# Optimization experiments

Hardware: AMD Instinct MI355X
Metric: run time of the kernel (lower is better)

The kernel has to match this reference:

```python
import jax, jax.numpy as jnp
import numpy as np

IN_FEATURES = 4096
OUT_FEATURES = 4096
LORA_R = 64
LORA_ALPHA = 16
SCALING = LORA_ALPHA / LORA_R  # 0.25


def setup_inputs() -> dict:
    key = jax.random.key(0)
    k_x, k_w, k_s, k_a, k_b = jax.random.split(key, 5)
    x = jax.random.normal(k_x, (4, 2048, IN_FEATURES), dtype=jnp.float32)
    # int8 quantized base weight in [-8, 7] as in the torch buffer init
    weight_quantized = jax.random.randint(k_w, (OUT_FEATURES, IN_FEATURES), -8, 7, dtype=jnp.int8)
    weight_scale = jax.random.normal(k_s, (1,), dtype=jnp.float32)
    lora_A = jax.random.normal(k_a, (LORA_R, IN_FEATURES), dtype=jnp.float32) * 0.01
    # torch init is zeros; use small random values so the LoRA path is exercised
    lora_B = jax.random.normal(k_b, (OUT_FEATURES, LORA_R), dtype=jnp.float32) * 0.01
    return {"x": x, "weight_quantized": weight_quantized, "weight_scale": weight_scale,
            "lora_A": lora_A, "lora_B": lora_B}


def reference(x, weight_quantized, weight_scale, lora_A, lora_B):
    # 1. dequantize base weight on the fly: [out, in]
    w_dequant = weight_quantized.astype(x.dtype) * weight_scale
    # 2. base GEMM: [B, S, in] x [in, out] -> [B, S, out]
    base = jnp.einsum('bsi,oi->bso', x, w_dequant)
    # 3. LoRA low-rank update (dropout is identity in eval mode)
    lora = jnp.einsum('bsr,or->bso', jnp.einsum('bsi,ri->bsr', x, lora_A), lora_B)
    return base + lora * SCALING
```

## Files before the change

### kernel.cpp

```cpp
#include <hip/hip_runtime.h>

#define M_TOT 8192
#define K_TOT 4096
#define N_TOT 4096
#define RANK  64
#define SCALING 0.25f

typedef __bf16 bf16x8 __attribute__((ext_vector_type(8)));
typedef float floatx4 __attribute__((ext_vector_type(4)));

static __device__ __forceinline__ unsigned short f32_to_bf16(float f) {
  unsigned int u = __float_as_uint(f);
  u += 0x7FFFu + ((u >> 16) & 1u);
  return (unsigned short)(u >> 16);
}

static __device__ __forceinline__ void async_ld16(const void* g, void* l) {
  __builtin_amdgcn_global_load_lds(
      (const __attribute__((address_space(1))) unsigned int*)g,
      (__attribute__((address_space(3))) unsigned int*)l, 16, 0, 0);
}

__global__ __launch_bounds__(256) void cvt_x_kernel(const float4* __restrict__ x,
                                                    ushort4* __restrict__ xb) {
  int i = blockIdx.x * 256 + threadIdx.x;
  float4 v = x[i];
  ushort4 o;
  o.x = f32_to_bf16(v.x);
  o.y = f32_to_bf16(v.y);
  o.z = f32_to_bf16(v.z);
  o.w = f32_to_bf16(v.w);
  xb[i] = o;
}

__global__ __launch_bounds__(256) void prep_kernel(
    const int* __restrict__ wq, const float* __restrict__ scale_p,
    const float* __restrict__ A, const float* __restrict__ B,
    unsigned short* __restrict__ Weff, unsigned short* __restrict__ Ab,
    unsigned short* __restrict__ Bb) {
  const int blk = blockIdx.x;
  const int tid = threadIdx.x;
  if (blk < 16384) {
    const float scale = scale_p[0];
    const size_t i = (size_t)(blk * 256 + tid) * 4;
    const int4 wv = *(const int4*)(wq + i);
    ushort4 st;
    st.x = f32_to_bf16((float)wv.x * scale);
    st.y = f32_to_bf16((float)wv.y * scale);
    st.z = f32_to_bf16((float)wv.z * scale);
    st.w = f32_to_bf16((float)wv.w * scale);
    *(ushort4*)(Weff + i) = st;
  } else if (blk < 16640) {
    const size_t i = (size_t)((blk - 16384) * 256 + tid) * 4;
    const float4 v = *(const float4*)(A + i);
    ushort4 st;
    st.x = f32_to_bf16(v.x);
    st.y = f32_to_bf16(v.y);
    st.z = f32_to_bf16(v.z);
    st.w = f32_to_bf16(v.w);
    *(ushort4*)(Ab + i) = st;
  } else {
    const size_t i = (size_t)((blk - 16640) * 256 + tid) * 4;
    const float4 v = *(const float4*)(B + i);
    ushort4 st;
    st.x = f32_to_bf16(v.x * SCALING);
    st.y = f32_to_bf16(v.y * SCALING);
    st.z = f32_to_bf16(v.z * SCALING);
    st.w = f32_to_bf16(v.w * SCALING);
    *(ushort4*)(Bb + i) = st;
  }
}

__global__ __launch_bounds__(256) void lora_y_kernel(
    const unsigned short* __restrict__ Xb,
    const unsigned short* __restrict__ Ab,
    unsigned short* __restrict__ Yb) {
  __shared__ __align__(16) unsigned short Xs[2 * 64 * 32];
  __shared__ __align__(16) unsigned short As[2 * 64 * 32];

  const int tid = threadIdx.x;
  const int lane = tid & 63;
  const int wave = tid >> 6;
  const int m0 = blockIdx.x * 64;

  const int sRow = tid >> 2;
  const int sCol = (tid & 3) * 8;
  const unsigned short* xg = Xb + (size_t)(m0 + sRow) * K_TOT + sCol;
  const unsigned short* ag = Ab + (size_t)sRow * K_TOT + sCol;
  unsigned short* lx0 = Xs + tid * 8;
  unsigned short* lx1 = Xs + 64 * 32 + tid * 8;
  unsigned short* la0 = As + tid * 8;
  unsigned short* la1 = As + 64 * 32 + tid * 8;

  const unsigned short* px = Xs + (wave * 16 + (lane & 15)) * 32 + (lane >> 4) * 8;
  const unsigned short* pav = As + (lane & 15) * 32 + (lane >> 4) * 8;

  floatx4 acc[4] = {};
  for (int kt = 0; kt < K_TOT; kt += 64) {
    __syncthreads();
    async_ld16(xg + kt, lx0);
    async_ld16(xg + kt + 32, lx1);
    async_ld16(ag + kt, la0);
    async_ld16(ag + kt + 32, la1);
    __syncthreads();
#pragma unroll
    for (int ks = 0; ks < 2; ++ks) {
      bf16x8 xf = *(const bf16x8*)(px + ks * 64 * 32);
#pragma unroll
      for (int j = 0; j < 4; ++j) {
        bf16x8 af = *(const bf16x8*)(pav + ks * 64 * 32 + j * 16 * 32);
        acc[j] = __builtin_amdgcn_mfma_f32_16x16x32_bf16(xf, af, acc[j], 0, 0, 0);
      }
    }
  }
  const int row0 = m0 + wave * 16 + ((lane >> 4) << 2);
  const int col0 = lane & 15;
#pragma unroll
  for (int j = 0; j < 4; ++j)
#pragma unroll
    for (int r = 0; r < 4; ++r)
      Yb[(size_t)(row0 + r) * RANK + (col0 + j * 16)] = f32_to_bf16(acc[j][r]);
}

__global__ __launch_bounds__(256) void gemm_kernel(
    const unsigned short* __restrict__ Xb,
    const unsigned short* __restrict__ Wb,
    const unsigned short* __restrict__ Yb,
    const unsigned short* __restrict__ Bb,
    float* __restrict__ out) {
  __shared__ __align__(16) unsigned short As[2 * 128 * 32];
  __shared__ __align__(16) unsigned short Bs[2 * 128 * 32];

  const int tid = threadIdx.x;
  const int lane = tid & 63;
  const int wave = tid >> 6;
  const int wm = wave >> 1;
  const int wn = wave & 1;

  const int bM = blockIdx.y * 128;
  const int bN = blockIdx.x * 128;

  const int sRow = tid >> 2;
  const int sCol = (tid & 3) * 8;
  const unsigned short* xg0 = Xb + (size_t)(bM + sRow) * K_TOT + sCol;
  const unsigned short* xg1 = xg0 + (size_t)64 * K_TOT;
  const unsigned short* wg0 = Wb + (size_t)(bN + sRow) * K_TOT + sCol;
  const unsigned short* wg1 = wg0 + (size_t)64 * K_TOT;
  unsigned short* la00 = As + tid * 8;
  unsigned short* la01 = As + 64 * 32 + tid * 8;
  unsigned short* la10 = As + 128 * 32 + tid * 8;
  unsigned short* la11 = As + 128 * 32 + 64 * 32 + tid * 8;
  unsigned short* lb00 = Bs + tid * 8;
  unsigned short* lb01 = Bs + 64 * 32 + tid * 8;
  unsigned short* lb10 = Bs + 128 * 32 + tid * 8;
  unsigned short* lb11 = Bs + 128 * 32 + 64 * 32 + tid * 8;

  const unsigned short* pa = As + ((wm * 64) + (lane & 15)) * 32 + (lane >> 4) * 8;
  const unsigned short* pb = Bs + ((wn * 64) + (lane & 15)) * 32 + (lane >> 4) * 8;

  floatx4 acc[4][4] = {};

  for (int kt = 0; kt < K_TOT; kt += 64) {
    __syncthreads();
    async_ld16(xg0 + kt, la00);
    async_ld16(xg1 + kt, la01);
    async_ld16(xg0 + kt + 32, la10);
    async_ld16(xg1 + kt + 32, la11);
    async_ld16(wg0 + kt, lb00);
    async_ld16(wg1 + kt, lb01);
    async_ld16(wg0 + kt + 32, lb10);
    async_ld16(wg1 + kt + 32, lb11);
    __syncthreads();

#pragma unroll
    for (int ks = 0; ks < 2; ++ks) {
      const unsigned short* pak = pa + ks * 128 * 32;
      const unsigned short* pbk = pb + ks * 128 * 32;
      bf16x8 af[4], bf[4];
#pragma unroll
      for (int i = 0; i < 4; ++i) af[i] = *(const bf16x8*)(pak + i * 16 * 32);
#pragma unroll
      for (int j = 0; j < 4; ++j) bf[j] = *(const bf16x8*)(pbk + j * 16 * 32);
#pragma unroll
      for (int i = 0; i < 4; ++i)
#pragma unroll
        for (int j = 0; j < 4; ++j)
          acc[i][j] = __builtin_amdgcn_mfma_f32_16x16x32_bf16(af[i], bf[j], acc[i][j], 0, 0, 0);
    }
  }

  {
    const unsigned short* yg0 = Yb + (size_t)(bM + sRow) * RANK + sCol;
    const unsigned short* yg1 = yg0 + (size_t)64 * RANK;
    const unsigned short* bg0 = Bb + (size_t)(bN + sRow) * RANK + sCol;
    const unsigned short* bg1 = bg0 + (size_t)64 * RANK;
    __syncthreads();
    async_ld16(yg0, la00);
    async_ld16(yg1, la01);
    async_ld16(yg0 + 32, la10);
    async_ld16(yg1 + 32, la11);
    async_ld16(bg0, lb00);
    async_ld16(bg1, lb01);
    async_ld16(bg0 + 32, lb10);
    async_ld16(bg1 + 32, lb11);
    __syncthreads();
#pragma unroll
    for (int ks = 0; ks < 2; ++ks) {
      const unsigned short* pak = pa + ks * 128 * 32;
      const unsigned short* pbk = pb + ks * 128 * 32;
      bf16x8 af[4], bf[4];
#pragma unroll
      for (int i = 0; i < 4; ++i) af[i] = *(const bf16x8*)(pak + i * 16 * 32);
#pragma unroll
      for (int j = 0; j < 4; ++j) bf[j] = *(const bf16x8*)(pbk + j * 16 * 32);
#pragma unroll
      for (int i = 0; i < 4; ++i)
#pragma unroll
        for (int j = 0; j < 4; ++j)
          acc[i][j] = __builtin_amdgcn_mfma_f32_16x16x32_bf16(af[i], bf[j], acc[i][j], 0, 0, 0);
    }
  }

  const int row0 = bM + wm * 64 + ((lane >> 4) << 2);
  const int col0 = bN + wn * 64 + (lane & 15);
#pragma unroll
  for (int i = 0; i < 4; ++i)
#pragma unroll
    for (int j = 0; j < 4; ++j)
#pragma unroll
      for (int r = 0; r < 4; ++r)
        out[(size_t)(row0 + i * 16 + r) * N_TOT + (col0 + j * 16)] = acc[i][j][r];
}

extern "C" void kernel_launch(void* const* d_in, const int* in_sizes, int n_in,
                              void* d_out, int out_size, void* d_ws, size_t ws_size,
                              hipStream_t stream) {
  const float* x      = (const float*)d_in[0];
  const int*   wq     = (const int*)d_in[1];
  const float* wscale = (const float*)d_in[2];
  const float* lora_A = (const float*)d_in[3];
  const float* lora_B = (const float*)d_in[4];
  float* out = (float*)d_out;

  char* ws = (char*)d_ws;
  unsigned short* xb   = (unsigned short*)(ws);
  unsigned short* weff = (unsigned short*)(ws + 67108864);
  unsigned short* yb   = (unsigned short*)(ws + 100663296);
  unsigned short* ab   = (unsigned short*)(ws + 101711872);
  unsigned short* bb   = (unsigned short*)(ws + 102236160);

  cvt_x_kernel<<<32768, 256, 0, stream>>>((const float4*)x, (ushort4*)xb);
  prep_kernel<<<16896, 256, 0, stream>>>(wq, wscale, lora_A, lora_B, weff, ab, bb);
  lora_y_kernel<<<128, 256, 0, stream>>>(xb, ab, yb);
  gemm_kernel<<<dim3(N_TOT / 128, M_TOT / 128), 256, 0, stream>>>(xb, weff, yb, bb, out);
}
```

Measured before the change: 606.2 us.

## Fuse x bf16 conversion into LoRA down-projection kernel and swizzle GEMM tiles

The standalone fp32-to-bf16 conversion of x is folded into the LoRA x·A^T kernel. That kernel now reads fp32 x once, converts it in registers, writes bf16 x to LDS and to global for the main GEMM, and prefetches the next chunk, which removes a separate 128MB read pass. The LoRA kernel uses 32-row tiles (256 blocks instead of 128) to spread work across more CUs. The main GEMM switches to a 1D grid with grouped tile ordering (32 M-tiles per group) to improve L2 reuse of the weight and x tiles. The fused kernel still runs only 256 blocks and its global stores are not async, so the conversion may be limited by that low parallelism.

New measurement: 596.4 us. Within noise of the previous version (-1.6%).

```diff
diff --git a/kernel.cpp b/kernel.cpp
--- a/kernel.cpp
+++ b/kernel.cpp
@@ -8,6 +8,7 @@
 
 typedef __bf16 bf16x8 __attribute__((ext_vector_type(8)));
 typedef float floatx4 __attribute__((ext_vector_type(4)));
+typedef unsigned short ushort8 __attribute__((ext_vector_type(8)));
 
 static __device__ __forceinline__ unsigned short f32_to_bf16(float f) {
   unsigned int u = __float_as_uint(f);
@@ -19,18 +20,6 @@
   __builtin_amdgcn_global_load_lds(
       (const __attribute__((address_space(1))) unsigned int*)g,
       (__attribute__((address_space(3))) unsigned int*)l, 16, 0, 0);
-}
-
-__global__ __launch_bounds__(256) void cvt_x_kernel(const float4* __restrict__ x,
-                                                    ushort4* __restrict__ xb) {
-  int i = blockIdx.x * 256 + threadIdx.x;
-  float4 v = x[i];
-  ushort4 o;
-  o.x = f32_to_bf16(v.x);
-  o.y = f32_to_bf16(v.y);
-  o.z = f32_to_bf16(v.z);
-  o.w = f32_to_bf16(v.w);
-  xb[i] = o;
 }
 
 __global__ __launch_bounds__(256) void prep_kernel(
@@ -71,52 +60,72 @@
   }
 }
 
-__global__ __launch_bounds__(256) void lora_y_kernel(
-    const unsigned short* __restrict__ Xb,
+__global__ __launch_bounds__(256) void cvt_lora_kernel(
+    const float* __restrict__ x,
     const unsigned short* __restrict__ Ab,
+    unsigned short* __restrict__ Xb,
     unsigned short* __restrict__ Yb) {
-  __shared__ __align__(16) unsigned short Xs[2 * 64 * 32];
+  __shared__ __align__(16) unsigned short Xs[2 * 32 * 32];
   __shared__ __align__(16) unsigned short As[2 * 64 * 32];
 
   const int tid = threadIdx.x;
   const int lane = tid & 63;
   const int wave = tid >> 6;
-  const int m0 = blockIdx.x * 64;
+  const int wm = wave & 1;
+  const int wn = wave >> 1;
+  const int m0 = blockIdx.x * 32;
+
+  const int xr = tid >> 3;
+  const int xc8 = (tid & 7) * 8;
+  const int xks = (tid & 7) >> 2;
+  const int xcin = xc8 & 31;
+  const float* xg = x + (size_t)(m0 + xr) * K_TOT + xc8;
+  unsigned short* xbg = Xb + (size_t)(m0 + xr) * K_TOT + xc8;
+  unsigned short* lx = Xs + xks * 1024 + xr * 32 + xcin;
 
   const int sRow = tid >> 2;
   const int sCol = (tid & 3) * 8;
-  const unsigned short* xg = Xb + (size_t)(m0 + sRow) * K_TOT + sCol;
   const unsigned short* ag = Ab + (size_t)sRow * K_TOT + sCol;
-  unsigned short* lx0 = Xs + tid * 8;
-  unsigned short* lx1 = Xs + 64 * 32 + tid * 8;
   unsigned short* la0 = As + tid * 8;
-  unsigned short* la1 = As + 64 * 32 + tid * 8;
-
-  const unsigned short* px = Xs + (wave * 16 + (lane & 15)) * 32 + (lane >> 4) * 8;
-  const unsigned short* pav = As + (lane & 15) * 32 + (lane >> 4) * 8;
-
-  floatx4 acc[4] = {};
+  unsigned short* la1 = As + 2048 + tid * 8;
+
+  const unsigned short* px = Xs + (wm * 16 + (lane & 15)) * 32 + (lane >> 4) * 8;
+  const unsigned short* pav = As + (wn * 32 + (lane & 15)) * 32 + (lane >> 4) * 8;
+
+  floatx4 acc[2] = {};
+
+  float4 v0 = *(const float4*)(xg);
+  float4 v1 = *(const float4*)(xg + 4);
   for (int kt = 0; kt < K_TOT; kt += 64) {
     __syncthreads();
-    async_ld16(xg + kt, lx0);
-    async_ld16(xg + kt + 32, lx1);
     async_ld16(ag + kt, la0);
     async_ld16(ag + kt + 32, la1);
+    ushort8 u;
+    u[0] = f32_to_bf16(v0.x); u[1] = f32_to_bf16(v0.y);
+    u[2] = f32_to_bf16(v0.z); u[3] = f32_to_bf16(v0.w);
+    u[4] = f32_to_bf16(v1.x); u[5] = f32_to_bf16(v1.y);
+    u[6] = f32_to_bf16(v1.z); u[7] = f32_to_bf16(v1.w);
+    *(ushort8*)lx = u;
+    *(ushort8*)(xbg + kt) = u;
+    if (kt + 64 < K_TOT) {
+      v0 = *(const float4*)(xg + kt + 64);
+      v1 = *(const float4*)(xg + kt + 68);
+    }
     __syncthreads();
 #pragma unroll
     for (int ks = 0; ks < 2; ++ks) {
-      bf16x8 xf = *(const bf16x8*)(px + ks * 64 * 32);
-#pragma unroll
-      for (int j = 0; j < 4; ++j) {
-        bf16x8 af = *(const bf16x8*)(pav + ks * 64 * 32 + j * 16 * 32);
+      bf16x8 xf = *(const bf16x8*)(px + ks * 1024);
+#pragma unroll
+      for (int j = 0; j < 2; ++j) {
+        bf16x8 af = *(const bf16x8*)(pav + ks * 2048 + j * 16 * 32);
         acc[j] = __builtin_amdgcn_mfma_f32_16x16x32_bf16(xf, af, acc[j], 0, 0, 0);
       }
     }
   }
-  const int row0 = m0 + wave * 16 + ((lane >> 4) << 2);
-  const int col0 = lane & 15;
-#pragma unroll
-  for (int j = 0; j < 4; ++j)
+  const int row0 = m0 + wm * 16 + ((lane >> 4) << 2);
+  const int col0 = wn * 32 + (lane & 15);
+#pragma unroll
+  for (int j = 0; j < 2; ++j)
 #pragma unroll
     for (int r = 0; r < 4; ++r)
       Yb[(size_t)(row0 + r) * RANK + (col0 + j * 16)] = f32_to_bf16(acc[j][r]);
@@ -137,8 +146,11 @@
   const int wm = wave >> 1;
   const int wn = wave & 1;
 
-  const int bM = blockIdx.y * 128;
-  const int bN = blockIdx.x * 128;
+  const int pid = blockIdx.x;
+  const int pid_m = ((pid >> 10) << 5) + (pid & 31);
+  const int pid_n = (pid & 1023) >> 5;
+  const int bM = pid_m * 128;
+  const int bN = pid_n * 128;
 
   const int sRow = tid >> 2;
   const int sCol = (tid & 3) * 8;
@@ -249,8 +261,7 @@
   unsigned short* ab   = (unsigned short*)(ws + 101711872);
   unsigned short* bb   = (unsigned short*)(ws + 102236160);
 
-  cvt_x_kernel<<<32768, 256, 0, stream>>>((const float4*)x, (ushort4*)xb);
   prep_kernel<<<16896, 256, 0, stream>>>(wq, wscale, lora_A, lora_B, weff, ab, bb);
-  lora_y_kernel<<<128, 256, 0, stream>>>(xb, ab, yb);
-  gemm_kernel<<<dim3(N_TOT / 128, M_TOT / 128), 256, 0, stream>>>(xb, weff, yb, bb, out);
-}
+  cvt_lora_kernel<<<256, 256, 0, stream>>>(x, ab, xb, yb);
+  gemm_kernel<<<2048, 256, 0, stream>>>(xb, weff, yb, bb, out);
+}
```
